# Optimization experiments

Hardware: AMD Instinct MI355X
Metric: run time of the kernel (lower is better)

## Reference

```python
import jax, jax.numpy as jnp
import numpy as np

B, N, D, H, L = 2, 2048, 512, 8, 2
HD = D // H


def setup_inputs() -> dict:
    key = jax.random.key(0)
    ks = jax.random.split(key, 8)
    s = 0.02
    return {
        "inputs_embeds": jax.random.normal(ks[0], (B, N, D), jnp.float32),
        "pos_emb": jax.random.normal(ks[1], (N, D), jnp.float32) * s,
        "c_attn_w": jax.random.normal(ks[2], (L, D, 3 * D), jnp.float32) * s,
        "c_attn_b": jnp.zeros((L, 3 * D), jnp.float32),
        "out_w": jax.random.normal(ks[3], (L, D, D), jnp.float32) * s,
        "out_b": jnp.zeros((L, D), jnp.float32),
        "ln1_g": jnp.ones((L, D), jnp.float32),
        "ln1_b": jnp.zeros((L, D), jnp.float32),
        "c_fc_w": jax.random.normal(ks[4], (L, D, 4 * D), jnp.float32) * s,
        "c_fc_b": jnp.zeros((L, 4 * D), jnp.float32),
        "c_proj_w": jax.random.normal(ks[5], (L, 4 * D, D), jnp.float32) * s,
        "c_proj_b": jnp.zeros((L, D), jnp.float32),
        "ln2_g": jnp.ones((L, D), jnp.float32),
        "ln2_b": jnp.zeros((L, D), jnp.float32),
    }


def _layernorm(x, g, b, eps=1e-5):
    mu = jnp.mean(x, axis=-1, keepdims=True)
    var = jnp.mean(jnp.square(x - mu), axis=-1, keepdims=True)
    return (x - mu) * jax.lax.rsqrt(var + eps) * g + b


def _gelu_new(x):
    # NewGELUActivation: tanh approximation
    return 0.5 * x * (1.0 + jnp.tanh(jnp.sqrt(2.0 / jnp.pi) * (x + 0.044715 * x ** 3)))


def _attention(x, w_qkv, b_qkv, w_out, b_out, self_mask):
    qkv = x @ w_qkv + b_qkv                      # [B,N,3D]
    q, k, v = jnp.split(qkv, 3, axis=-1)
    def heads(t):
        return t.reshape(B, N, H, HD).transpose(0, 2, 1, 3)  # [B,H,N,HD]
    q, k, v = heads(q), heads(k), heads(v)
    scores = jnp.einsum('bhqd,bhkd->bhqk', q, k) / jnp.sqrt(jnp.float32(HD))
    neg = jnp.finfo(scores.dtype).min
    scores = jnp.where(self_mask, scores, neg)   # exclude-self mask
    attn = jax.nn.softmax(scores, axis=-1)
    o = jnp.einsum('bhqk,bhkd->bhqd', attn, v)
    o = o.transpose(0, 2, 1, 3).reshape(B, N, D)
    return o @ w_out + b_out


def reference(inputs_embeds, pos_emb, c_attn_w, c_attn_b, out_w, out_b,
              ln1_g, ln1_b, c_fc_w, c_fc_b, c_proj_w, c_proj_b, ln2_g, ln2_b):
    self_mask = ~jnp.eye(N, dtype=bool)[None, None]  # [1,1,N,N]
    h = inputs_embeds + pos_emb[None]
    for l in range(L):
        res = h
        x = _layernorm(h, ln1_g[l], ln1_b[l])
        h = _attention(x, c_attn_w[l], c_attn_b[l], out_w[l], out_b[l], self_mask) + res
        res = h
        x = _layernorm(h, ln2_g[l], ln2_b[l])
        x = _gelu_new(x @ c_fc_w[l] + c_fc_b[l])
        h = (x @ c_proj_w[l] + c_proj_b[l]) + res
    return h
```

## Files before the change

### kernel.cpp

```cpp
#include <hip/hip_runtime.h>
#include <hip/hip_bf16.h>
#include <math.h>

#define BB 2
#define NN 2048
#define DD 512
#define HH 8
#define LL 2
#define TT (BB*NN)

typedef short short8 __attribute__((ext_vector_type(8)));
typedef float floatx4 __attribute__((ext_vector_type(4)));

__device__ __forceinline__ unsigned short f2b(float v) {
    union { float f; unsigned u; } x; x.f = v;
    unsigned r = x.u + 0x7fff + ((x.u >> 16) & 1);
    return (unsigned short)(r >> 16);
}

__device__ __forceinline__ void gld16(const unsigned short* g, unsigned short* lds) {
    __builtin_amdgcn_global_load_lds(
        (const __attribute__((address_space(1))) unsigned int*)g,
        (__attribute__((address_space(3))) unsigned int*)lds,
        16, 0, 0);
}

__global__ __launch_bounds__(256) void k_bias_add(const float* __restrict__ src,
                                                  const float* __restrict__ bias,
                                                  float* __restrict__ dst) {
    int i = blockIdx.x * 256 + threadIdx.x;
    dst[i] = src[i] + bias[i & (DD - 1)];
}

template <int EMB>
__global__ __launch_bounds__(256) void k_ln(const float* __restrict__ hin,
                                            unsigned short* __restrict__ xout,
                                            const float* __restrict__ g,
                                            const float* __restrict__ b,
                                            const float* __restrict__ emb,
                                            const float* __restrict__ pos,
                                            float* __restrict__ hout) {
    __shared__ float red[4];
    __shared__ float bc1, bc2;
    int t = blockIdx.x;
    int tid = threadIdx.x;
    int lane = tid & 63, wv = tid >> 6;
    float v0, v1;
    if (EMB) {
        const float* erow = emb + (size_t)t * DD;
        const float* prow = pos + (size_t)(t & (NN - 1)) * DD;
        v0 = erow[tid] + prow[tid];
        v1 = erow[tid + 256] + prow[tid + 256];
        hout[(size_t)t * DD + tid] = v0;
        hout[(size_t)t * DD + tid + 256] = v1;
    } else {
        const float* row = hin + (size_t)t * DD;
        v0 = row[tid];
        v1 = row[tid + 256];
    }

    float s = v0 + v1;
#pragma unroll
    for (int o = 32; o; o >>= 1) s += __shfl_down(s, o, 64);
    if (lane == 0) red[wv] = s;
    __syncthreads();
    if (tid == 0) bc1 = (red[0] + red[1] + red[2] + red[3]) * (1.0f / DD);
    __syncthreads();
    float mu = bc1;
    float d0 = v0 - mu, d1 = v1 - mu;
    s = d0 * d0 + d1 * d1;
#pragma unroll
    for (int o = 32; o; o >>= 1) s += __shfl_down(s, o, 64);
    if (lane == 0) red[wv] = s;
    __syncthreads();
    if (tid == 0) bc2 = (red[0] + red[1] + red[2] + red[3]) * (1.0f / DD);
    __syncthreads();
    float rstd = rsqrtf(bc2 + 1e-5f);
    xout[(size_t)t * DD + tid]       = f2b(d0 * rstd * g[tid] + b[tid]);
    xout[(size_t)t * DD + tid + 256] = f2b(d1 * rstd * g[tid + 256] + b[tid + 256]);
}

__device__ __forceinline__ float gelu_new(float v) {
    const float c = 0.7978845608028654f;
    float u = c * (v + 0.044715f * v * v * v);
    u = fminf(fmaxf(u, -30.0f), 30.0f);
    float e = __builtin_amdgcn_exp2f(2.885390081777927f * u);
    return v * e * __builtin_amdgcn_rcpf(e + 1.0f);
}

#define PL 3145728
__global__ __launch_bounds__(256) void k_wt_all(const float* __restrict__ c_attn_w,
                                                const float* __restrict__ out_w,
                                                const float* __restrict__ c_fc_w,
                                                const float* __restrict__ c_proj_w,
                                                unsigned short* __restrict__ wbuf) {
    __shared__ unsigned short t[64][72];
    int bx = blockIdx.x;
    int l = bx / 768;
    int r = bx - l * 768;
    const float* W; unsigned short* WT; int K, N;
    if (r < 192)      { W = c_attn_w + (size_t)l * 512 * 1536; WT = wbuf + (size_t)l * PL;           K = 512;  N = 1536; }
    else if (r < 256) { r -= 192; W = out_w  + (size_t)l * 512 * 512;  WT = wbuf + (size_t)l * PL + 786432;  K = 512;  N = 512; }
    else if (r < 512) { r -= 256; W = c_fc_w + (size_t)l * 512 * 2048; WT = wbuf + (size_t)l * PL + 1048576; K = 512;  N = 2048; }
    else              { r -= 512; W = c_proj_w + (size_t)l * 2048 * 512; WT = wbuf + (size_t)l * PL + 2097152; K = 2048; N = 512; }
    int tiles_n = N >> 6;
    int n0 = (r % tiles_n) * 64, k0 = (r / tiles_n) * 64;

    int tid = threadIdx.x;
    int rr = tid >> 2;
    int c0 = (tid & 3) * 16;
    const float* src = W + (size_t)(k0 + rr) * N + n0 + c0;
#pragma unroll
    for (int u = 0; u < 4; u++) {
        float4 v = *(const float4*)&src[u * 4];
        t[c0 + u * 4 + 0][rr] = f2b(v.x);
        t[c0 + u * 4 + 1][rr] = f2b(v.y);
        t[c0 + u * 4 + 2][rr] = f2b(v.z);
        t[c0 + u * 4 + 3][rr] = f2b(v.w);
    }
    __syncthreads();
    unsigned short* dst = WT + (size_t)(n0 + rr) * K + k0 + c0;
#pragma unroll
    for (int u = 0; u < 4; u++)
        *(uint2*)&dst[u * 4] = *(const uint2*)&t[rr][c0 + u * 4];
}

template <int ACT, int BF16OUT, int ATOMIC>
__global__ __launch_bounds__(512) void k_mgemm(const unsigned short* __restrict__ Ab,
                                               const unsigned short* __restrict__ Bt,
                                               const float* __restrict__ bias,
                                               float* __restrict__ Cp,
                                               unsigned short* __restrict__ Cb,
                                               int Kfull, int Kchunk, int N) {
    __shared__ unsigned short Als[2][8 * 512];
    __shared__ unsigned short Bls[2][8 * 512];

    int tid = threadIdx.x;
    int l = tid & 63, w = tid >> 6;
    int wm = w >> 2, wn = w & 3;
    int m0 = blockIdx.y * 128, n0 = blockIdx.x * 128;
    int kb = blockIdx.z * Kchunk;
    int lr = l & 15;
    int lk = (l >> 4) * 8;

    const unsigned short* Ap = Ab + (size_t)(m0 + w * 16 + lr) * Kfull + kb + lk;
    const unsigned short* Bp = Bt + (size_t)(n0 + w * 16 + lr) * Kfull + kb + lk;
    unsigned short* lsA = &Als[0][0];
    unsigned short* lsB = &Bls[0][0];
    int wbase = w << 9;

    floatx4 acc[4][2];
#pragma unroll
    for (int i = 0; i < 4; i++)
#pragma unroll
        for (int j = 0; j < 2; j++) acc[i][j] = (floatx4){0.f, 0.f, 0.f, 0.f};

    int nit = Kchunk >> 5;

    gld16(Ap, lsA + wbase);
    gld16(Bp, lsB + wbase);
    __syncthreads();

    for (int it = 0; it < nit; it++) {
        int c = it & 1;
        if (it + 1 < nit) {
            int ko = (it + 1) << 5;
            int db = (c ^ 1) << 12;
            gld16(Ap + ko, lsA + db + wbase);
            gld16(Bp + ko, lsB + db + wbase);
        }
        short8 a[4], b[2];
        int cb = c << 12;
#pragma unroll
        for (int i = 0; i < 4; i++)
            a[i] = *(const short8*)&lsA[cb + (wm * 4 + i) * 512 + l * 8];
#pragma unroll
        for (int j = 0; j < 2; j++)
            b[j] = *(const short8*)&lsB[cb + (wn * 2 + j) * 512 + l * 8];
#pragma unroll
        for (int i = 0; i < 4; i++)
#pragma unroll
            for (int j = 0; j < 2; j++)
                acc[i][j] = __builtin_amdgcn_mfma_f32_16x16x32_bf16(a[i], b[j], acc[i][j], 0, 0, 0);
        __syncthreads();
    }

    int col_in = l & 15, rquad = (l >> 4) * 4;
    bool addb = (!ATOMIC) || (bias != nullptr && blockIdx.z == 0);
#pragma unroll
    for (int i = 0; i < 4; i++) {
        int gm_base = m0 + wm * 64 + i * 16 + rquad;
#pragma unroll
        for (int j = 0; j < 2; j++) {
            int gn = n0 + wn * 32 + j * 16 + col_in;
            float bv = addb ? bias[gn] : 0.0f;
#pragma unroll
            for (int r = 0; r < 4; r++) {
                size_t off = (size_t)(gm_base + r) * N + gn;
                if (ATOMIC) {
                    atomicAdd(&Cp[off], acc[i][j][r] + bv);
                } else {
                    float v = acc[i][j][r] + bv;
                    if (ACT) v = gelu_new(v);
                    if (BF16OUT) Cb[off] = f2b(v);
                    else Cp[off] = v;
                }
            }
        }
    }
}

__global__ __launch_bounds__(256) void k_attn_mfma(const unsigned short* __restrict__ qkv,
                                                   unsigned short* __restrict__ xatt) {
    __shared__ unsigned short Ks[2][64 * 72];
    __shared__ unsigned short Vt[2][64 * 72];
    __shared__ unsigned short Pls[64 * 72];

    int qt = blockIdx.x, hd = blockIdx.y, b = blockIdx.z;
    int tid = threadIdx.x;
    int l = tid & 63, w = tid >> 6;
    int lr = l & 15, quad = l >> 4;

    const size_t base = (size_t)b * NN * 1536;

    short8 qf[2];
    {
        const unsigned short* qrow = qkv + base + (size_t)(qt * 64 + w * 16 + lr) * 1536 + hd * 64;
        qf[0] = *(const short8*)&qrow[quad * 8];
        qf[1] = *(const short8*)&qrow[quad * 8 + 32];
    }

    floatx4 O[4];
#pragma unroll
    for (int jd = 0; jd < 4; jd++) O[jd] = (floatx4){0.f, 0.f, 0.f, 0.f};
    float lsum = 0.0f;

    int sr = tid >> 2, sc = (tid & 3) * 16;
    int vk = (tid & 15) * 4, vd = (tid >> 4) * 4;
    const int STEP = 64 * 1536;
    const unsigned short* Kp = qkv + base + 512 + hd * 64 + (size_t)sr * 1536 + sc;
    const unsigned short* Vp = qkv + base + 1024 + hd * 64 + (size_t)vk * 1536 + vd;

    uint4 rk0, rk1;
    union { uint2 u; unsigned short s[4]; } rv[4];

    rk0 = *(const uint4*)Kp;
    rk1 = *(const uint4*)(Kp + 8);
#pragma unroll
    for (int i = 0; i < 4; i++)
        rv[i].u = *(const uint2*)(Vp + (size_t)i * 1536);
    *(uint4*)&Ks[0][sr * 72 + sc]     = rk0;
    *(uint4*)&Ks[0][sr * 72 + sc + 8] = rk1;
#pragma unroll
    for (int j = 0; j < 4; j++) {
        union { uint2 u; unsigned short s[4]; } pk;
        pk.s[0] = rv[0].s[j]; pk.s[1] = rv[1].s[j];
        pk.s[2] = rv[2].s[j]; pk.s[3] = rv[3].s[j];
        *(uint2*)&Vt[0][(vd + j) * 72 + vk] = pk.u;
    }
    Kp += STEP; Vp += STEP;
    rk0 = *(const uint4*)Kp;
    rk1 = *(const uint4*)(Kp + 8);
#pragma unroll
    for (int i = 0; i < 4; i++)
        rv[i].u = *(const uint2*)(Vp + (size_t)i * 1536);
    __syncthreads();

    const float EC1 = 0.18033688011112042f;
    const float EC0 = -11.541560327111707f;

    for (int kt = 0; kt < 32; kt++) {
        int c = kt & 1;

        floatx4 s[4];
#pragma unroll
        for (int jn = 0; jn < 4; jn++) s[jn] = (floatx4){0.f, 0.f, 0.f, 0.f};
#pragma unroll
        for (int ss = 0; ss < 2; ss++)
#pragma unroll
            for (int jn = 0; jn < 4; jn++) {
                short8 ak = *(const short8*)&Ks[c][(jn * 16 + lr) * 72 + ss * 32 + quad * 8];
                s[jn] = __builtin_amdgcn_mfma_f32_16x16x32_bf16(ak, qf[ss], s[jn], 0, 0, 0);
            }

        int mq = w * 16 + lr;
        bool diag = (kt == qt);
#pragma unroll
        for (int jn = 0; jn < 4; jn++) {
            float p0 = __builtin_amdgcn_exp2f(fmaf(s[jn][0], EC1, EC0));
            float p1 = __builtin_amdgcn_exp2f(fmaf(s[jn][1], EC1, EC0));
            float p2 = __builtin_amdgcn_exp2f(fmaf(s[jn][2], EC1, EC0));
            float p3 = __builtin_amdgcn_exp2f(fmaf(s[jn][3], EC1, EC0));
            if (diag) {
                int kbase = jn * 16 + quad * 4;
                if (mq == kbase + 0) p0 = 0.0f;
                if (mq == kbase + 1) p1 = 0.0f;
                if (mq == kbase + 2) p2 = 0.0f;
                if (mq == kbase + 3) p3 = 0.0f;
            }
            lsum += (p0 + p1) + (p2 + p3);
            unsigned w01, w23;
            asm("v_cvt_pk_bf16_f32 %0, %1, %2" : "=v"(w01) : "v"(p0), "v"(p1));
            asm("v_cvt_pk_bf16_f32 %0, %1, %2" : "=v"(w23) : "v"(p2), "v"(p3));
            uint2 pku; pku.x = w01; pku.y = w23;
            *(uint2*)&Pls[mq * 72 + jn * 16 + quad * 4] = pku;
        }

#pragma unroll
        for (int ss = 0; ss < 2; ss++) {
            short8 ap = *(const short8*)&Pls[(w * 16 + lr) * 72 + ss * 32 + quad * 8];
#pragma unroll
            for (int jd = 0; jd < 4; jd++) {
                short8 bv = *(const short8*)&Vt[c][(jd * 16 + lr) * 72 + ss * 32 + quad * 8];
                O[jd] = __builtin_amdgcn_mfma_f32_16x16x32_bf16(ap, bv, O[jd], 0, 0, 0);
            }
        }

        if (kt < 31) {
            *(uint4*)&Ks[c ^ 1][sr * 72 + sc]     = rk0;
            *(uint4*)&Ks[c ^ 1][sr * 72 + sc + 8] = rk1;
#pragma unroll
            for (int j = 0; j < 4; j++) {
                union { uint2 u; unsigned short s[4]; } pk;
                pk.s[0] = rv[0].s[j]; pk.s[1] = rv[1].s[j];
                pk.s[2] = rv[2].s[j]; pk.s[3] = rv[3].s[j];
                *(uint2*)&Vt[c ^ 1][(vd + j) * 72 + vk] = pk.u;
            }
            if (kt < 30) {
                Kp += STEP; Vp += STEP;
                rk0 = *(const uint4*)Kp;
                rk1 = *(const uint4*)(Kp + 8);
#pragma unroll
                for (int i = 0; i < 4; i++)
                    rv[i].u = *(const uint2*)(Vp + (size_t)i * 1536);
            }
        }
        __syncthreads();
    }

    lsum += __shfl_xor(lsum, 16);
    lsum += __shfl_xor(lsum, 32);
#pragma unroll
    for (int r = 0; r < 4; r++) {
        float inv = 1.0f / __shfl(lsum, quad * 4 + r, 16);
        size_t tok = (size_t)b * NN + qt * 64 + w * 16 + quad * 4 + r;
#pragma unroll
        for (int jd = 0; jd < 4; jd++)
            xatt[tok * DD + hd * 64 + jd * 16 + lr] = f2b(O[jd][r] * inv);
    }
}

extern "C" void kernel_launch(void* const* d_in, const int* in_sizes, int n_in,
                              void* d_out, int out_size, void* d_ws, size_t ws_size,
                              hipStream_t stream) {
    const float* emb      = (const float*)d_in[0];
    const float* pos      = (const float*)d_in[1];
    const float* c_attn_w = (const float*)d_in[2];
    const float* c_attn_b = (const float*)d_in[3];
    const float* out_w    = (const float*)d_in[4];
    const float* out_b    = (const float*)d_in[5];
    const float* ln1_g    = (const float*)d_in[6];
    const float* ln1_b    = (const float*)d_in[7];
    const float* c_fc_w   = (const float*)d_in[8];
    const float* c_fc_b   = (const float*)d_in[9];
    const float* c_proj_w = (const float*)d_in[10];
    const float* c_proj_b = (const float*)d_in[11];
    const float* ln2_g    = (const float*)d_in[12];
    const float* ln2_b    = (const float*)d_in[13];

    char* p = (char*)d_ws;
    float* h = (float*)p;                       p += (size_t)TT * DD * 4;
    unsigned short* act = (unsigned short*)p;   p += (size_t)TT * 2048 * 2;
    unsigned short* x = (unsigned short*)p;     p += (size_t)TT * DD * 2;
    unsigned short* xatt = (unsigned short*)p;  p += (size_t)TT * DD * 2;
    unsigned short* wbuf = (unsigned short*)p;

    unsigned short* qkvb = act;
    unsigned short* ffa  = act;
    float* out = (float*)d_out;

    k_wt_all<<<1536, 256, 0, stream>>>(c_attn_w, out_w, c_fc_w, c_proj_w, wbuf);

    for (int l = 0; l < LL; l++) {
        unsigned short* wqkv_t  = wbuf + (size_t)l * PL;
        unsigned short* wout_t  = wqkv_t + 786432;
        unsigned short* wfc_t   = wqkv_t + 1048576;
        unsigned short* wproj_t = wqkv_t + 2097152;

        if (l == 0)
            k_ln<1><<<TT, 256, 0, stream>>>(nullptr, x, ln1_g, ln1_b, emb, pos, h);
        else
            k_ln<0><<<TT, 256, 0, stream>>>(h, x, ln1_g + l * DD, ln1_b + l * DD,
                                            nullptr, nullptr, nullptr);
        k_mgemm<0, 1, 0><<<dim3(1536 / 128, TT / 128), 512, 0, stream>>>(
            x, wqkv_t, c_attn_b + l * 1536, nullptr, qkvb, 512, 512, 1536);
        k_attn_mfma<<<dim3(NN / 64, HH, BB), 256, 0, stream>>>(qkvb, xatt);
        k_mgemm<0, 0, 1><<<dim3(512 / 128, TT / 128, 2), 512, 0, stream>>>(
            xatt, wout_t, out_b + l * DD, h, nullptr, 512, 256, 512);
        k_ln<0><<<TT, 256, 0, stream>>>(h, x, ln2_g + l * DD, ln2_b + l * DD,
                                        nullptr, nullptr, nullptr);
        k_mgemm<1, 1, 0><<<dim3(2048 / 128, TT / 128), 512, 0, stream>>>(
            x, wfc_t, c_fc_b + l * 2048, nullptr, ffa, 512, 512, 2048);
        if (l == LL - 1) {
            k_bias_add<<<TT * DD / 256, 256, 0, stream>>>(h, c_proj_b + l * DD, out);
            k_mgemm<0, 0, 1><<<dim3(512 / 128, TT / 128, 4), 512, 0, stream>>>(
                ffa, wproj_t, nullptr, out, nullptr, 2048, 512, 512);
        } else {
            k_mgemm<0, 0, 1><<<dim3(512 / 128, TT / 128, 4), 512, 0, stream>>>(
                ffa, wproj_t, c_proj_b + l * DD, h, nullptr, 2048, 512, 512);
        }
    }
}
```

Before: 414.0 us.

## Software-pipeline attention: overlap previous tile's PV MFMA with current QK scores

Restructures the attention loop so each iteration issues the P·V MFMAs for the previous key tile right after the current tile's Q·K MFMAs, before the exp/softmax work. P is double-buffered and V is triple-buffered in LDS so the lagging tile's data survives one extra iteration. The last tile's P·V is drained after the loop. This aims to hide exp and bf16-pack latency behind matrix-core work. The cost is more LDS per block (about 64KB instead of 46KB), which may reduce the number of resident blocks per CU.

```diff
diff --git a/kernel.cpp b/kernel.cpp
--- a/kernel.cpp
+++ b/kernel.cpp
@@ -213,8 +213,8 @@
 __global__ __launch_bounds__(256) void k_attn_mfma(const unsigned short* __restrict__ qkv,
                                                    unsigned short* __restrict__ xatt) {
     __shared__ unsigned short Ks[2][64 * 72];
-    __shared__ unsigned short Vt[2][64 * 72];
-    __shared__ unsigned short Pls[64 * 72];
+    __shared__ unsigned short Vt[3][64 * 72];
+    __shared__ unsigned short Pls[2][64 * 72];
 
     int qt = blockIdx.x, hd = blockIdx.y, b = blockIdx.z;
     int tid = threadIdx.x;
@@ -269,8 +269,12 @@
     const float EC1 = 0.18033688011112042f;
     const float EC0 = -11.541560327111707f;
 
+    int mq = w * 16 + lr;
+
     for (int kt = 0; kt < 32; kt++) {
-        int c = kt & 1;
+        int ck = kt & 1;
+        int v_pv = (kt + 2) % 3;
+        int v_st = (kt + 1) % 3;
 
         floatx4 s[4];
 #pragma unroll
@@ -279,11 +283,22 @@
         for (int ss = 0; ss < 2; ss++)
 #pragma unroll
             for (int jn = 0; jn < 4; jn++) {
-                short8 ak = *(const short8*)&Ks[c][(jn * 16 + lr) * 72 + ss * 32 + quad * 8];
+                short8 ak = *(const short8*)&Ks[ck][(jn * 16 + lr) * 72 + ss * 32 + quad * 8];
                 s[jn] = __builtin_amdgcn_mfma_f32_16x16x32_bf16(ak, qf[ss], s[jn], 0, 0, 0);
             }
 
-        int mq = w * 16 + lr;
+        if (kt > 0) {
+#pragma unroll
+            for (int ss = 0; ss < 2; ss++) {
+                short8 ap = *(const short8*)&Pls[ck ^ 1][(w * 16 + lr) * 72 + ss * 32 + quad * 8];
+#pragma unroll
+                for (int jd = 0; jd < 4; jd++) {
+                    short8 bv = *(const short8*)&Vt[v_pv][(jd * 16 + lr) * 72 + ss * 32 + quad * 8];
+                    O[jd] = __builtin_amdgcn_mfma_f32_16x16x32_bf16(ap, bv, O[jd], 0, 0, 0);
+                }
+            }
+        }
+
         bool diag = (kt == qt);
 #pragma unroll
         for (int jn = 0; jn < 4; jn++) {
@@ -303,28 +318,18 @@
             asm("v_cvt_pk_bf16_f32 %0, %1, %2" : "=v"(w01) : "v"(p0), "v"(p1));
             asm("v_cvt_pk_bf16_f32 %0, %1, %2" : "=v"(w23) : "v"(p2), "v"(p3));
             uint2 pku; pku.x = w01; pku.y = w23;
-            *(uint2*)&Pls[mq * 72 + jn * 16 + quad * 4] = pku;
-        }
-
-#pragma unroll
-        for (int ss = 0; ss < 2; ss++) {
-            short8 ap = *(const short8*)&Pls[(w * 16 + lr) * 72 + ss * 32 + quad * 8];
-#pragma unroll
-            for (int jd = 0; jd < 4; jd++) {
-                short8 bv = *(const short8*)&Vt[c][(jd * 16 + lr) * 72 + ss * 32 + quad * 8];
-                O[jd] = __builtin_amdgcn_mfma_f32_16x16x32_bf16(ap, bv, O[jd], 0, 0, 0);
-            }
+            *(uint2*)&Pls[ck][mq * 72 + jn * 16 + quad * 4] = pku;
         }
 
         if (kt < 31) {
-            *(uint4*)&Ks[c ^ 1][sr * 72 + sc]     = rk0;
-            *(uint4*)&Ks[c ^ 1][sr * 72 + sc + 8] = rk1;
+            *(uint4*)&Ks[ck ^ 1][sr * 72 + sc]     = rk0;
+            *(uint4*)&Ks[ck ^ 1][sr * 72 + sc + 8] = rk1;
 #pragma unroll
             for (int j = 0; j < 4; j++) {
                 union { uint2 u; unsigned short s[4]; } pk;
                 pk.s[0] = rv[0].s[j]; pk.s[1] = rv[1].s[j];
                 pk.s[2] = rv[2].s[j]; pk.s[3] = rv[3].s[j];
-                *(uint2*)&Vt[c ^ 1][(vd + j) * 72 + vk] = pk.u;
+                *(uint2*)&Vt[v_st][(vd + j) * 72 + vk] = pk.u;
             }
             if (kt < 30) {
                 Kp += STEP; Vp += STEP;
@@ -336,6 +341,16 @@
             }
         }
         __syncthreads();
+    }
+
+#pragma unroll
+    for (int ss = 0; ss < 2; ss++) {
+        short8 ap = *(const short8*)&Pls[1][(w * 16 + lr) * 72 + ss * 32 + quad * 8];
+#pragma unroll
+        for (int jd = 0; jd < 4; jd++) {
+            short8 bv = *(const short8*)&Vt[1][(jd * 16 + lr) * 72 + ss * 32 + quad * 8];
+            O[jd] = __builtin_amdgcn_mfma_f32_16x16x32_bf16(ap, bv, O[jd], 0, 0, 0);
+        }
     }
 
     lsum += __shfl_xor(lsum, 16);
```

Result: no change. 416.3 us (+0.6%).
